# Performance work log

Hardware: AMD Instinct MI355X
Metric: run time of the kernel (lower is better)

Reference implementation:

```python
import jax, jax.numpy as jnp
import numpy as np

HEADS = 4
DIM_HEAD = 32
DIM = 128

def _layernorm(x, g, b, eps=1e-5):
    mu = x.mean(-1, keepdims=True)
    var = ((x - mu) ** 2).mean(-1, keepdims=True)
    return (x - mu) / jnp.sqrt(var + eps) * g + b

def setup_inputs() -> dict:
    key = jax.random.key(0)
    ks = jax.random.split(key, 12)
    d = {}
    d['q'] = jax.random.normal(ks[0], (1, 6, 8, 8, 16, 16, DIM), jnp.float32)
    d['k'] = jax.random.normal(ks[1], (1, 6, 8, 8, 6, 6, DIM), jnp.float32)
    d['v'] = jax.random.normal(ks[2], (1, 6, 8, 8, 6, 6, DIM), jnp.float32)
    d['skip'] = jax.random.normal(ks[3], (1, 8, 8, 16, 16, DIM), jnp.float32)
    inner = HEADS * DIM_HEAD
    # LayerNorm params for to_q/to_k/to_v pre-norms
    d['gq'] = jnp.ones((DIM,), jnp.float32); d['bq_ln'] = jnp.zeros((DIM,), jnp.float32)
    d['gk'] = jnp.ones((DIM,), jnp.float32); d['bk_ln'] = jnp.zeros((DIM,), jnp.float32)
    d['gv'] = jnp.ones((DIM,), jnp.float32); d['bv_ln'] = jnp.zeros((DIM,), jnp.float32)
    # Linear weights stored (in, out)
    d['Wq'] = jax.random.normal(ks[4], (DIM, inner), jnp.float32) * 0.02
    d['bq'] = jnp.zeros((inner,), jnp.float32)
    d['Wk'] = jax.random.normal(ks[5], (DIM, inner), jnp.float32) * 0.02
    d['bk'] = jnp.zeros((inner,), jnp.float32)
    d['Wv'] = jax.random.normal(ks[6], (DIM, inner), jnp.float32) * 0.02
    d['bv'] = jnp.zeros((inner,), jnp.float32)
    d['Wp'] = jax.random.normal(ks[7], (inner, DIM), jnp.float32) * 0.02
    d['bp'] = jnp.zeros((DIM,), jnp.float32)
    return d

def _window_flat(t):
    # (b n x y w1 w2 d) -> (b, x*y, n*w1*w2, d)
    b, n, gx, gy, wh, ww, d = t.shape
    t = jnp.transpose(t, (0, 2, 3, 1, 4, 5, 6))
    return t.reshape(b, gx * gy, n * wh * ww, d)

def reference(q, k, v, skip, gq, bq_ln, gk, bk_ln, gv, bv_ln, Wq, bq, Wk, bk, Wv, bv, Wp, bp):
    B, N, X, Y, W1, W2, D = q.shape
    scale = DIM_HEAD ** -0.5
    qf = _window_flat(q)  # (B, L, Qn, D), L = X*Y
    kf = _window_flat(k)  # (B, L, Kn, D)
    vf = _window_flat(v)
    L, Qn = qf.shape[1], qf.shape[2]
    Kn = kf.shape[2]
    qh = (_layernorm(qf, gq, bq_ln) @ Wq + bq).reshape(B, L, Qn, HEADS, DIM_HEAD)
    kh = (_layernorm(kf, gk, bk_ln) @ Wk + bk).reshape(B, L, Kn, HEADS, DIM_HEAD)
    vh = (_layernorm(vf, gv, bv_ln) @ Wv + bv).reshape(B, L, Kn, HEADS, DIM_HEAD)
    dot = jnp.einsum('blqhd,blkhd->bhlqk', qh, kh) * scale
    att = jax.nn.softmax(dot, axis=-1)
    a = jnp.einsum('bhlqk,blkhd->blqhd', att, vh).reshape(B, L, Qn, HEADS * DIM_HEAD)
    z = a @ Wp + bp  # (B, L, Qn, D)
    # back to (B, N, X, Y, W1, W2, D)
    z = z.reshape(B, X, Y, N, W1, W2, D)
    z = jnp.transpose(z, (0, 3, 1, 2, 4, 5, 6))
    z = z.mean(axis=1)  # pool over views -> (B, X, Y, W1, W2, D)
    return z + skip
```

## Files before the change

kernel.cpp:

```cpp
#include <hip/hip_runtime.h>

typedef __attribute__((ext_vector_type(8))) short bf16x8;
typedef __attribute__((ext_vector_type(4))) float f32x4;

__device__ __forceinline__ unsigned short f2bf(float f) {
  unsigned u = __builtin_bit_cast(unsigned, f);
  return (unsigned short)((u + 0x7fffu + ((u >> 16) & 1u)) >> 16);
}

__global__ __launch_bounds__(256) void prep_kernel(const float* __restrict__ W,
                                                   unsigned short* __restrict__ Wt) {
  int i = blockIdx.x * 256 + threadIdx.x;
  int k = i >> 7, n = i & 127;
  Wt[n * 128 + k] = f2bf(W[i]);
}

template <int WW>
__global__ __launch_bounds__(256) void ln_proj_kernel(
    const float* __restrict__ src,
    const float* __restrict__ gamma, const float* __restrict__ beta,
    const unsigned short* __restrict__ Wt,
    const float* __restrict__ bias, float outscale,
    unsigned short* __restrict__ dst) {
  __shared__ __align__(16) unsigned short xs[64][136];
  __shared__ __align__(16) unsigned short wsm[128][136];
  const int tid = threadIdx.x;
  const int base = blockIdx.x * 64;

  {
    const uint4* Wt4 = (const uint4*)Wt;
    for (int i = tid; i < 2048; i += 256)
      *(uint4*)&wsm[i >> 4][(i & 15) * 8] = Wt4[i];
  }

  const int tok = tid >> 2, part = tid & 3;
  {
    const float* x = src + (size_t)(base + tok) * 128 + part * 32;
    float v[32];
    float s = 0.f;
#pragma unroll
    for (int i = 0; i < 8; i++) {
      float4 f = ((const float4*)x)[i];
      v[4 * i] = f.x; v[4 * i + 1] = f.y; v[4 * i + 2] = f.z; v[4 * i + 3] = f.w;
      s += f.x + f.y + f.z + f.w;
    }
    s += __shfl_xor(s, 1); s += __shfl_xor(s, 2);
    const float mu = s * (1.f / 128.f);
    float vs = 0.f;
#pragma unroll
    for (int i = 0; i < 32; i++) { float d = v[i] - mu; vs += d * d; }
    vs += __shfl_xor(vs, 1); vs += __shfl_xor(vs, 2);
    const float rstd = rsqrtf(vs * (1.f / 128.f) + 1e-5f);
#pragma unroll
    for (int i = 0; i < 32; i++) {
      int d = part * 32 + i;
      xs[tok][d] = f2bf((v[i] - mu) * rstd * gamma[d] + beta[d]);
    }
  }
  __syncthreads();

  const int lane = tid & 63, wv = tid >> 6;
  const int lr = lane & 15, lg = lane >> 4;
  bf16x8 af[4];
#pragma unroll
  for (int ks = 0; ks < 4; ks++)
    af[ks] = *(const bf16x8*)&xs[wv * 16 + lr][ks * 32 + lg * 8];
  f32x4 acc[8];
#pragma unroll
  for (int nt = 0; nt < 8; nt++) {
    f32x4 a = {0.f, 0.f, 0.f, 0.f};
#pragma unroll
    for (int ks = 0; ks < 4; ks++) {
      bf16x8 bf = *(const bf16x8*)&wsm[nt * 16 + lr][ks * 32 + lg * 8];
      a = __builtin_amdgcn_mfma_f32_16x16x32_bf16(af[ks], bf, a, 0, 0, 0);
    }
    acc[nt] = a;
  }
  __syncthreads();
#pragma unroll
  for (int nt = 0; nt < 8; nt++) {
    const int n = nt * 16 + lr;
    const float b = bias[n];
#pragma unroll
    for (int rr = 0; rr < 4; rr++)
      xs[wv * 16 + lg * 4 + rr][n] = f2bf((acc[nt][rr] + b) * outscale);
  }
  __syncthreads();
  for (int i = tid; i < 1024; i += 256) {
    const int row = i >> 4, c8 = i & 15;
    const int sr = base + row;
    const int p = sr % WW;
    const int t1 = sr / WW;
    const int yy = t1 & 7;
    const int t2 = t1 >> 3;
    const int xx = t2 & 7;
    const int nn = t2 >> 3;
    const int dr = ((xx * 8 + yy) * 6 + nn) * WW + p;
    *(uint4*)(dst + (size_t)dr * 128 + c8 * 8) = *(const uint4*)&xs[row][c8 * 8];
  }
}

__global__ __launch_bounds__(512) void attn_kernel(
    const unsigned short* __restrict__ qh,
    const unsigned short* __restrict__ kh,
    const unsigned short* __restrict__ vh,
    float* __restrict__ abar) {
  __shared__ __align__(16) unsigned short Kl[224][40];
  __shared__ __align__(16) unsigned short Vt[32][232];
  __shared__ __align__(16) unsigned short P[8][16][248];
  const int tid = threadIdx.x;
  const int h = blockIdx.x, l = blockIdx.y;

  const unsigned short* kb = kh + (size_t)l * 216 * 128 + h * 32;
  for (int i = tid; i < 864; i += 512) {
    const int key = i >> 2, c = i & 3;
    *(uint4*)&Kl[key][c * 8] = *(const uint4*)&kb[(size_t)key * 128 + c * 8];
  }
  const unsigned short* vb = vh + (size_t)l * 216 * 128 + h * 32;
  for (int i = tid; i < 864; i += 512) {
    const int key = i >> 2, c = i & 3;
    uint4 d = *(const uint4*)&vb[(size_t)key * 128 + c * 8];
    const unsigned short* e = (const unsigned short*)&d;
#pragma unroll
    for (int j = 0; j < 8; j++) Vt[c * 8 + j][key] = e[j];
  }
  if (tid < 32) { uint4 z = {0, 0, 0, 0}; *(uint4*)&Vt[tid][216] = z; }
  __syncthreads();

  const int w = tid >> 6, lane = tid & 63;
  const int lr = lane & 15, lg = lane >> 4;

  for (int pt2 = 0; pt2 < 2; ++pt2) {
    const int pt = w * 2 + pt2;
    f32x4 acc[2] = {{0.f, 0.f, 0.f, 0.f}, {0.f, 0.f, 0.f, 0.f}};
#pragma unroll
    for (int wv = 0; wv < 6; ++wv) {
      const bf16x8 qf = *(const bf16x8*)
          &qh[((size_t)l * 1536 + wv * 256 + pt * 16 + lr) * 128 + h * 32 + lg * 8];

      f32x4 sc[14];
#pragma unroll
      for (int kt = 0; kt < 14; kt++) {
        bf16x8 kf = *(const bf16x8*)&Kl[kt * 16 + lr][lg * 8];
        f32x4 z = {0.f, 0.f, 0.f, 0.f};
        sc[kt] = __builtin_amdgcn_mfma_f32_16x16x32_bf16(kf, qf, z, 0, 0, 0);
      }
      if (lg >= 2) {
        sc[13][0] = -3e38f; sc[13][1] = -3e38f; sc[13][2] = -3e38f; sc[13][3] = -3e38f;
      }
      float sum = 0.f;
#pragma unroll
      for (int kt = 0; kt < 14; kt++)
#pragma unroll
        for (int rr = 0; rr < 4; rr++) {
          float e = __builtin_amdgcn_exp2f(sc[kt][rr]);
          sc[kt][rr] = e;
          sum += e;
        }
      sum += __shfl_xor(sum, 16);
      sum += __shfl_xor(sum, 32);
      const float inv = __builtin_amdgcn_rcpf(sum);

#pragma unroll
      for (int kt = 0; kt < 14; kt++) {
        unsigned r0, r1;
        asm("v_cvt_pk_bf16_f32 %0, %1, %2" : "=v"(r0) : "v"(sc[kt][0]), "v"(sc[kt][1]));
        asm("v_cvt_pk_bf16_f32 %0, %1, %2" : "=v"(r1) : "v"(sc[kt][2]), "v"(sc[kt][3]));
        uint2 wr; wr.x = r0; wr.y = r1;
        *(uint2*)&P[w][lr][kt * 16 + lg * 4] = wr;
      }

      f32x4 tmp[2] = {{0.f, 0.f, 0.f, 0.f}, {0.f, 0.f, 0.f, 0.f}};
#pragma unroll
      for (int s = 0; s < 7; s++) {
        bf16x8 pa = *(const bf16x8*)&P[w][lr][s * 32 + lg * 8];
#pragma unroll
        for (int nt = 0; nt < 2; nt++) {
          bf16x8 vf = *(const bf16x8*)&Vt[nt * 16 + lr][s * 32 + lg * 8];
          tmp[nt] = __builtin_amdgcn_mfma_f32_16x16x32_bf16(pa, vf, tmp[nt], 0, 0, 0);
        }
      }
#pragma unroll
      for (int rr = 0; rr < 4; rr++) {
        const float invq = __shfl(inv, lg * 4 + rr);
        acc[0][rr] += tmp[0][rr] * invq;
        acc[1][rr] += tmp[1][rr] * invq;
      }
    }
#pragma unroll
    for (int nt = 0; nt < 2; nt++)
#pragma unroll
      for (int rr = 0; rr < 4; rr++)
        abar[((size_t)l * 256 + pt * 16 + lg * 4 + rr) * 128 + h * 32 + nt * 16 + lr] =
            acc[nt][rr] * (1.f / 6.f);
  }
}

__global__ __launch_bounds__(256) void out_proj_kernel(
    const float* __restrict__ abar,
    const unsigned short* __restrict__ Wt,
    const float* __restrict__ bias,
    const float* __restrict__ skip,
    float* __restrict__ out) {
  __shared__ __align__(16) unsigned short xs[64][136];
  __shared__ __align__(16) unsigned short wsm[128][136];
  const int tid = threadIdx.x;
  const size_t base = (size_t)blockIdx.x * 64;
  {
    const uint4* Wt4 = (const uint4*)Wt;
    for (int i = tid; i < 2048; i += 256)
      *(uint4*)&wsm[i >> 4][(i & 15) * 8] = Wt4[i];
  }
  const int tok = tid >> 2, part = tid & 3;
  {
    const float* x = abar + (base + tok) * 128 + part * 32;
#pragma unroll
    for (int i = 0; i < 8; i++) {
      float4 f = ((const float4*)x)[i];
      unsigned short* o = &xs[tok][part * 32 + i * 4];
      o[0] = f2bf(f.x); o[1] = f2bf(f.y); o[2] = f2bf(f.z); o[3] = f2bf(f.w);
    }
  }
  __syncthreads();
  const int lane = tid & 63, wv = tid >> 6;
  const int lr = lane & 15, lg = lane >> 4;
  bf16x8 af[4];
#pragma unroll
  for (int ks = 0; ks < 4; ks++)
    af[ks] = *(const bf16x8*)&xs[wv * 16 + lr][ks * 32 + lg * 8];
#pragma unroll
  for (int nt = 0; nt < 8; nt++) {
    f32x4 a = {0.f, 0.f, 0.f, 0.f};
#pragma unroll
    for (int ks = 0; ks < 4; ks++) {
      bf16x8 bf = *(const bf16x8*)&wsm[nt * 16 + lr][ks * 32 + lg * 8];
      a = __builtin_amdgcn_mfma_f32_16x16x32_bf16(af[ks], bf, a, 0, 0, 0);
    }
    const int n = nt * 16 + lr;
    const float b = bias[n];
#pragma unroll
    for (int rr = 0; rr < 4; rr++) {
      const size_t row = base + wv * 16 + lg * 4 + rr;
      out[row * 128 + n] = a[rr] + b + skip[row * 128 + n];
    }
  }
}

extern "C" void kernel_launch(void* const* d_in, const int* in_sizes, int n_in,
                              void* d_out, int out_size, void* d_ws, size_t ws_size,
                              hipStream_t stream) {
  const float* q     = (const float*)d_in[0];
  const float* k     = (const float*)d_in[1];
  const float* v     = (const float*)d_in[2];
  const float* skip  = (const float*)d_in[3];
  const float* gq    = (const float*)d_in[4];
  const float* bq_ln = (const float*)d_in[5];
  const float* gk    = (const float*)d_in[6];
  const float* bk_ln = (const float*)d_in[7];
  const float* gv    = (const float*)d_in[8];
  const float* bv_ln = (const float*)d_in[9];
  const float* Wq    = (const float*)d_in[10];
  const float* bq    = (const float*)d_in[11];
  const float* Wk    = (const float*)d_in[12];
  const float* bk    = (const float*)d_in[13];
  const float* Wv    = (const float*)d_in[14];
  const float* bv    = (const float*)d_in[15];
  const float* Wp    = (const float*)d_in[16];
  const float* bp    = (const float*)d_in[17];

  char* w = (char*)d_ws;
  unsigned short* WtQ = (unsigned short*)(w);
  unsigned short* WtK = (unsigned short*)(w + 32768);
  unsigned short* WtV = (unsigned short*)(w + 65536);
  unsigned short* WtP = (unsigned short*)(w + 98304);
  unsigned short* qhb = (unsigned short*)(w + 131072);
  unsigned short* khb = (unsigned short*)(w + 131072 + 25165824);
  unsigned short* vhb = (unsigned short*)(w + 131072 + 25165824 + 3538944);
  float* abar         = (float*)(w + 131072 + 25165824 + 2 * 3538944);

  prep_kernel<<<64, 256, 0, stream>>>(Wq, WtQ);
  prep_kernel<<<64, 256, 0, stream>>>(Wk, WtK);
  prep_kernel<<<64, 256, 0, stream>>>(Wv, WtV);
  prep_kernel<<<64, 256, 0, stream>>>(Wp, WtP);

  const float scale = 0.17677669529663687f * 1.4426950408889634f;
  ln_proj_kernel<256><<<1536, 256, 0, stream>>>(q, gq, bq_ln, WtQ, bq, scale, qhb);
  ln_proj_kernel<36><<<216, 256, 0, stream>>>(k, gk, bk_ln, WtK, bk, 1.f, khb);
  ln_proj_kernel<36><<<216, 256, 0, stream>>>(v, gv, bv_ln, WtV, bv, 1.f, vhb);

  attn_kernel<<<dim3(4, 64), 512, 0, stream>>>(qhb, khb, vhb, abar);
  out_proj_kernel<<<256, 256, 0, stream>>>(abar, WtP, bp, skip, (float*)d_out);
}
```

Measured before the change: 92.24 us.

## Load LN/proj inputs straight into MFMA registers, enlarge blocks, prefetch Q in attention

After: 83.10 us. 9.9% less time.

```diff
diff --git a/kernel.cpp b/kernel.cpp
--- a/kernel.cpp
+++ b/kernel.cpp
@@ -6,6 +6,11 @@
 __device__ __forceinline__ unsigned short f2bf(float f) {
   unsigned u = __builtin_bit_cast(unsigned, f);
   return (unsigned short)((u + 0x7fffu + ((u >> 16) & 1u)) >> 16);
+}
+__device__ __forceinline__ unsigned pk2bf(float a, float b) {
+  unsigned r;
+  asm("v_cvt_pk_bf16_f32 %0, %1, %2" : "=v"(r) : "v"(a), "v"(b));
+  return r;
 }
 
 __global__ __launch_bounds__(256) void prep_kernel(const float* __restrict__ W,
@@ -16,55 +21,68 @@
 }
 
 template <int WW>
-__global__ __launch_bounds__(256) void ln_proj_kernel(
+__global__ __launch_bounds__(512, 4) void ln_proj_kernel(
     const float* __restrict__ src,
     const float* __restrict__ gamma, const float* __restrict__ beta,
     const unsigned short* __restrict__ Wt,
     const float* __restrict__ bias, float outscale,
     unsigned short* __restrict__ dst) {
-  __shared__ __align__(16) unsigned short xs[64][136];
+  __shared__ __align__(16) unsigned short xs[128][136];
   __shared__ __align__(16) unsigned short wsm[128][136];
   const int tid = threadIdx.x;
-  const int base = blockIdx.x * 64;
+  const int base = blockIdx.x * 128;
 
   {
     const uint4* Wt4 = (const uint4*)Wt;
-    for (int i = tid; i < 2048; i += 256)
+    for (int i = tid; i < 2048; i += 512)
       *(uint4*)&wsm[i >> 4][(i & 15) * 8] = Wt4[i];
   }
 
-  const int tok = tid >> 2, part = tid & 3;
+  const int w = tid >> 6, lane = tid & 63;
+  const int lr = lane & 15, lg = lane >> 4;
+  const int row = base + w * 16 + lr;
+
+  float v[32];
+  float s = 0.f;
   {
-    const float* x = src + (size_t)(base + tok) * 128 + part * 32;
-    float v[32];
-    float s = 0.f;
-#pragma unroll
-    for (int i = 0; i < 8; i++) {
-      float4 f = ((const float4*)x)[i];
-      v[4 * i] = f.x; v[4 * i + 1] = f.y; v[4 * i + 2] = f.z; v[4 * i + 3] = f.w;
-      s += f.x + f.y + f.z + f.w;
-    }
-    s += __shfl_xor(s, 1); s += __shfl_xor(s, 2);
-    const float mu = s * (1.f / 128.f);
-    float vs = 0.f;
-#pragma unroll
-    for (int i = 0; i < 32; i++) { float d = v[i] - mu; vs += d * d; }
-    vs += __shfl_xor(vs, 1); vs += __shfl_xor(vs, 2);
-    const float rstd = rsqrtf(vs * (1.f / 128.f) + 1e-5f);
-#pragma unroll
-    for (int i = 0; i < 32; i++) {
-      int d = part * 32 + i;
-      xs[tok][d] = f2bf((v[i] - mu) * rstd * gamma[d] + beta[d]);
-    }
+    const float* x = src + (size_t)row * 128 + lg * 8;
+#pragma unroll
+    for (int ks = 0; ks < 4; ks++)
+#pragma unroll
+      for (int j = 0; j < 2; j++) {
+        float4 f = *(const float4*)(x + ks * 32 + j * 4);
+        v[ks * 8 + j * 4 + 0] = f.x; v[ks * 8 + j * 4 + 1] = f.y;
+        v[ks * 8 + j * 4 + 2] = f.z; v[ks * 8 + j * 4 + 3] = f.w;
+        s += f.x + f.y + f.z + f.w;
+      }
+  }
+  s += __shfl_xor(s, 16); s += __shfl_xor(s, 32);
+  const float mu = s * (1.f / 128.f);
+  float vs = 0.f;
+#pragma unroll
+  for (int i = 0; i < 32; i++) { float d = v[i] - mu; vs += d * d; }
+  vs += __shfl_xor(vs, 16); vs += __shfl_xor(vs, 32);
+  const float rstd = rsqrtf(vs * (1.f / 128.f) + 1e-5f);
+
+  bf16x8 af[4];
+#pragma unroll
+  for (int ks = 0; ks < 4; ks++) {
+    unsigned pk[4];
+#pragma unroll
+    for (int j = 0; j < 2; j++) {
+      float4 g = *(const float4*)(gamma + ks * 32 + lg * 8 + j * 4);
+      float4 b = *(const float4*)(beta + ks * 32 + lg * 8 + j * 4);
+      float o0 = (v[ks * 8 + j * 4 + 0] - mu) * rstd * g.x + b.x;
+      float o1 = (v[ks * 8 + j * 4 + 1] - mu) * rstd * g.y + b.y;
+      float o2 = (v[ks * 8 + j * 4 + 2] - mu) * rstd * g.z + b.z;
+      float o3 = (v[ks * 8 + j * 4 + 3] - mu) * rstd * g.w + b.w;
+      pk[j * 2 + 0] = pk2bf(o0, o1);
+      pk[j * 2 + 1] = pk2bf(o2, o3);
+    }
+    af[ks] = __builtin_bit_cast(bf16x8, *(uint4*)pk);
   }
   __syncthreads();
 
-  const int lane = tid & 63, wv = tid >> 6;
-  const int lr = lane & 15, lg = lane >> 4;
-  bf16x8 af[4];
-#pragma unroll
-  for (int ks = 0; ks < 4; ks++)
-    af[ks] = *(const bf16x8*)&xs[wv * 16 + lr][ks * 32 + lg * 8];
   f32x4 acc[8];
 #pragma unroll
   for (int nt = 0; nt < 8; nt++) {
@@ -76,19 +94,18 @@
     }
     acc[nt] = a;
   }
-  __syncthreads();
 #pragma unroll
   for (int nt = 0; nt < 8; nt++) {
     const int n = nt * 16 + lr;
     const float b = bias[n];
 #pragma unroll
     for (int rr = 0; rr < 4; rr++)
-      xs[wv * 16 + lg * 4 + rr][n] = f2bf((acc[nt][rr] + b) * outscale);
+      xs[w * 16 + lg * 4 + rr][n] = f2bf((acc[nt][rr] + b) * outscale);
   }
   __syncthreads();
-  for (int i = tid; i < 1024; i += 256) {
-    const int row = i >> 4, c8 = i & 15;
-    const int sr = base + row;
+  for (int i = tid; i < 2048; i += 512) {
+    const int r = i >> 4, c8 = i & 15;
+    const int sr = base + r;
     const int p = sr % WW;
     const int t1 = sr / WW;
     const int yy = t1 & 7;
@@ -96,104 +113,107 @@
     const int xx = t2 & 7;
     const int nn = t2 >> 3;
     const int dr = ((xx * 8 + yy) * 6 + nn) * WW + p;
-    *(uint4*)(dst + (size_t)dr * 128 + c8 * 8) = *(const uint4*)&xs[row][c8 * 8];
-  }
-}
-
-__global__ __launch_bounds__(512) void attn_kernel(
+    *(uint4*)(dst + (size_t)dr * 128 + c8 * 8) = *(const uint4*)&xs[r][c8 * 8];
+  }
+}
+
+__global__ __launch_bounds__(1024) void attn_kernel(
     const unsigned short* __restrict__ qh,
     const unsigned short* __restrict__ kh,
     const unsigned short* __restrict__ vh,
     float* __restrict__ abar) {
   __shared__ __align__(16) unsigned short Kl[224][40];
   __shared__ __align__(16) unsigned short Vt[32][232];
-  __shared__ __align__(16) unsigned short P[8][16][248];
+  __shared__ __align__(16) unsigned short P[16][16][232];
   const int tid = threadIdx.x;
   const int h = blockIdx.x, l = blockIdx.y;
 
-  const unsigned short* kb = kh + (size_t)l * 216 * 128 + h * 32;
-  for (int i = tid; i < 864; i += 512) {
-    const int key = i >> 2, c = i & 3;
+  if (tid < 864) {
+    const unsigned short* kb = kh + (size_t)l * 216 * 128 + h * 32;
+    const int key = tid >> 2, c = tid & 3;
     *(uint4*)&Kl[key][c * 8] = *(const uint4*)&kb[(size_t)key * 128 + c * 8];
-  }
-  const unsigned short* vb = vh + (size_t)l * 216 * 128 + h * 32;
-  for (int i = tid; i < 864; i += 512) {
-    const int key = i >> 2, c = i & 3;
+    const unsigned short* vb = vh + (size_t)l * 216 * 128 + h * 32;
     uint4 d = *(const uint4*)&vb[(size_t)key * 128 + c * 8];
     const unsigned short* e = (const unsigned short*)&d;
 #pragma unroll
     for (int j = 0; j < 8; j++) Vt[c * 8 + j][key] = e[j];
   }
-  if (tid < 32) { uint4 z = {0, 0, 0, 0}; *(uint4*)&Vt[tid][216] = z; }
+  if (tid >= 960) { uint4 z = {0, 0, 0, 0}; *(uint4*)&Vt[tid - 960][216] = z; }
   __syncthreads();
 
   const int w = tid >> 6, lane = tid & 63;
   const int lr = lane & 15, lg = lane >> 4;
-
-  for (int pt2 = 0; pt2 < 2; ++pt2) {
-    const int pt = w * 2 + pt2;
-    f32x4 acc[2] = {{0.f, 0.f, 0.f, 0.f}, {0.f, 0.f, 0.f, 0.f}};
-#pragma unroll
-    for (int wv = 0; wv < 6; ++wv) {
-      const bf16x8 qf = *(const bf16x8*)
-          &qh[((size_t)l * 1536 + wv * 256 + pt * 16 + lr) * 128 + h * 32 + lg * 8];
-
-      f32x4 sc[14];
-#pragma unroll
-      for (int kt = 0; kt < 14; kt++) {
-        bf16x8 kf = *(const bf16x8*)&Kl[kt * 16 + lr][lg * 8];
-        f32x4 z = {0.f, 0.f, 0.f, 0.f};
-        sc[kt] = __builtin_amdgcn_mfma_f32_16x16x32_bf16(kf, qf, z, 0, 0, 0);
+  const int pt = w;
+
+  const unsigned short* qbase =
+      qh + ((size_t)l * 1536 + pt * 16 + lr) * 128 + h * 32 + lg * 8;
+
+  f32x4 acc[2] = {{0.f, 0.f, 0.f, 0.f}, {0.f, 0.f, 0.f, 0.f}};
+  bf16x8 qf = *(const bf16x8*)qbase;
+#pragma unroll
+  for (int wv = 0; wv < 6; ++wv) {
+    bf16x8 qnext;
+    if (wv < 5) qnext = *(const bf16x8*)(qbase + (size_t)(wv + 1) * 256 * 128);
+
+    f32x4 sc[14];
+    __builtin_amdgcn_s_setprio(1);
+#pragma unroll
+    for (int kt = 0; kt < 14; kt++) {
+      bf16x8 kf = *(const bf16x8*)&Kl[kt * 16 + lr][lg * 8];
+      f32x4 z = {0.f, 0.f, 0.f, 0.f};
+      sc[kt] = __builtin_amdgcn_mfma_f32_16x16x32_bf16(kf, qf, z, 0, 0, 0);
+    }
+    __builtin_amdgcn_s_setprio(0);
+    if (lg >= 2) {
+      sc[13][0] = -3e38f; sc[13][1] = -3e38f; sc[13][2] = -3e38f; sc[13][3] = -3e38f;
+    }
+    float sum = 0.f;
+#pragma unroll
+    for (int kt = 0; kt < 14; kt++)
+#pragma unroll
+      for (int rr = 0; rr < 4; rr++) {
+        float e = __builtin_amdgcn_exp2f(sc[kt][rr]);
+        sc[kt][rr] = e;
+        sum += e;
       }
-      if (lg >= 2) {
-        sc[13][0] = -3e38f; sc[13][1] = -3e38f; sc[13][2] = -3e38f; sc[13][3] = -3e38f;
+    sum += __shfl_xor(sum, 16);
+    sum += __shfl_xor(sum, 32);
+    const float inv = __builtin_amdgcn_rcpf(sum) * (1.f / 6.f);
+
+#pragma unroll
+    for (int kt = 0; kt < 14; kt++) {
+      uint2 wr;
+      wr.x = pk2bf(sc[kt][0], sc[kt][1]);
+      wr.y = pk2bf(sc[kt][2], sc[kt][3]);
+      *(uint2*)&P[w][lr][kt * 16 + lg * 4] = wr;
+    }
+
+    f32x4 tmp[2] = {{0.f, 0.f, 0.f, 0.f}, {0.f, 0.f, 0.f, 0.f}};
+    __builtin_amdgcn_s_setprio(1);
+#pragma unroll
+    for (int s = 0; s < 7; s++) {
+      bf16x8 pa = *(const bf16x8*)&P[w][lr][s * 32 + lg * 8];
+#pragma unroll
+      for (int nt = 0; nt < 2; nt++) {
+        bf16x8 vf = *(const bf16x8*)&Vt[nt * 16 + lr][s * 32 + lg * 8];
+        tmp[nt] = __builtin_amdgcn_mfma_f32_16x16x32_bf16(pa, vf, tmp[nt], 0, 0, 0);
       }
-      float sum = 0.f;
-#pragma unroll
-      for (int kt = 0; kt < 14; kt++)
-#pragma unroll
-        for (int rr = 0; rr < 4; rr++) {
-          float e = __builtin_amdgcn_exp2f(sc[kt][rr]);
-          sc[kt][rr] = e;
-          sum += e;
-        }
-      sum += __shfl_xor(sum, 16);
-      sum += __shfl_xor(sum, 32);
-      const float inv = __builtin_amdgcn_rcpf(sum);
-
-#pragma unroll
-      for (int kt = 0; kt < 14; kt++) {
-        unsigned r0, r1;
-        asm("v_cvt_pk_bf16_f32 %0, %1, %2" : "=v"(r0) : "v"(sc[kt][0]), "v"(sc[kt][1]));
-        asm("v_cvt_pk_bf16_f32 %0, %1, %2" : "=v"(r1) : "v"(sc[kt][2]), "v"(sc[kt][3]));
-        uint2 wr; wr.x = r0; wr.y = r1;
-        *(uint2*)&P[w][lr][kt * 16 + lg * 4] = wr;
-      }
-
-      f32x4 tmp[2] = {{0.f, 0.f, 0.f, 0.f}, {0.f, 0.f, 0.f, 0.f}};
-#pragma unroll
-      for (int s = 0; s < 7; s++) {
-        bf16x8 pa = *(const bf16x8*)&P[w][lr][s * 32 + lg * 8];
-#pragma unroll
-        for (int nt = 0; nt < 2; nt++) {
-          bf16x8 vf = *(const bf16x8*)&Vt[nt * 16 + lr][s * 32 + lg * 8];
-          tmp[nt] = __builtin_amdgcn_mfma_f32_16x16x32_bf16(pa, vf, tmp[nt], 0, 0, 0);
-        }
-      }
-#pragma unroll
-      for (int rr = 0; rr < 4; rr++) {
-        const float invq = __shfl(inv, lg * 4 + rr);
-        acc[0][rr] += tmp[0][rr] * invq;
-        acc[1][rr] += tmp[1][rr] * invq;
-      }
-    }
-#pragma unroll
-    for (int nt = 0; nt < 2; nt++)
-#pragma unroll
-      for (int rr = 0; rr < 4; rr++)
-        abar[((size_t)l * 256 + pt * 16 + lg * 4 + rr) * 128 + h * 32 + nt * 16 + lr] =
-            acc[nt][rr] * (1.f / 6.f);
-  }
+    }
+    __builtin_amdgcn_s_setprio(0);
+#pragma unroll
+    for (int rr = 0; rr < 4; rr++) {
+      const float invq = __shfl(inv, lg * 4 + rr);
+      acc[0][rr] += tmp[0][rr] * invq;
+      acc[1][rr] += tmp[1][rr] * invq;
+    }
+    qf = qnext;
+  }
+#pragma unroll
+  for (int nt = 0; nt < 2; nt++)
+#pragma unroll
+    for (int rr = 0; rr < 4; rr++)
+      abar[((size_t)l * 256 + pt * 16 + lg * 4 + rr) * 128 + h * 32 + nt * 16 + lr] =
+          acc[nt][rr];
 }
 
 __global__ __launch_bounds__(256) void out_proj_kernel(
@@ -202,7 +222,6 @@
     const float* __restrict__ bias,
     const float* __restrict__ skip,
     float* __restrict__ out) {
-  __shared__ __align__(16) unsigned short xs[64][136];
   __shared__ __align__(16) unsigned short wsm[128][136];
   const int tid = threadIdx.x;
   const size_t base = (size_t)blockIdx.x * 64;
@@ -211,23 +230,23 @@
     for (int i = tid; i < 2048; i += 256)
       *(uint4*)&wsm[i >> 4][(i & 15) * 8] = Wt4[i];
   }
-  const int tok = tid >> 2, part = tid & 3;
+  const int lane = tid & 63, w = tid >> 6;
+  const int lr = lane & 15, lg = lane >> 4;
+  const size_t row = base + w * 16 + lr;
+  bf16x8 af[4];
   {
-    const float* x = abar + (base + tok) * 128 + part * 32;
-#pragma unroll
-    for (int i = 0; i < 8; i++) {
-      float4 f = ((const float4*)x)[i];
-      unsigned short* o = &xs[tok][part * 32 + i * 4];
-      o[0] = f2bf(f.x); o[1] = f2bf(f.y); o[2] = f2bf(f.z); o[3] = f2bf(f.w);
+    const float* x = abar + row * 128 + lg * 8;
+#pragma unroll
+    for (int ks = 0; ks < 4; ks++) {
+      float4 f0 = *(const float4*)(x + ks * 32);
+      float4 f1 = *(const float4*)(x + ks * 32 + 4);
+      unsigned pk[4];
+      pk[0] = pk2bf(f0.x, f0.y); pk[1] = pk2bf(f0.z, f0.w);
+      pk[2] = pk2bf(f1.x, f1.y); pk[3] = pk2bf(f1.z, f1.w);
+      af[ks] = __builtin_bit_cast(bf16x8, *(uint4*)pk);
     }
   }
   __syncthreads();
-  const int lane = tid & 63, wv = tid >> 6;
-  const int lr = lane & 15, lg = lane >> 4;
-  bf16x8 af[4];
-#pragma unroll
-  for (int ks = 0; ks < 4; ks++)
-    af[ks] = *(const bf16x8*)&xs[wv * 16 + lr][ks * 32 + lg * 8];
 #pragma unroll
   for (int nt = 0; nt < 8; nt++) {
     f32x4 a = {0.f, 0.f, 0.f, 0.f};
@@ -240,8 +259,8 @@
     const float b = bias[n];
 #pragma unroll
     for (int rr = 0; rr < 4; rr++) {
-      const size_t row = base + wv * 16 + lg * 4 + rr;
-      out[row * 128 + n] = a[rr] + b + skip[row * 128 + n];
+      const size_t r = base + w * 16 + lg * 4 + rr;
+      out[r * 128 + n] = a[rr] + b + skip[r * 128 + n];
     }
   }
 }
@@ -284,10 +303,10 @@
   prep_kernel<<<64, 256, 0, stream>>>(Wp, WtP);
 
   const float scale = 0.17677669529663687f * 1.4426950408889634f;
-  ln_proj_kernel<256><<<1536, 256, 0, stream>>>(q, gq, bq_ln, WtQ, bq, scale, qhb);
-  ln_proj_kernel<36><<<216, 256, 0, stream>>>(k, gk, bk_ln, WtK, bk, 1.f, khb);
-  ln_proj_kernel<36><<<216, 256, 0, stream>>>(v, gv, bv_ln, WtV, bv, 1.f, vhb);
-
-  attn_kernel<<<dim3(4, 64), 512, 0, stream>>>(qhb, khb, vhb, abar);
+  ln_proj_kernel<256><<<768, 512, 0, stream>>>(q, gq, bq_ln, WtQ, bq, scale, qhb);
+  ln_proj_kernel<36><<<108, 512, 0, stream>>>(k, gk, bk_ln, WtK, bk, 1.f, khb);
+  ln_proj_kernel<36><<<108, 512, 0, stream>>>(v, gv, bv_ln, WtV, bv, 1.f, vhb);
+
+  attn_kernel<<<dim3(4, 64), 1024, 0, stream>>>(qhb, khb, vhb, abar);
   out_proj_kernel<<<256, 256, 0, stream>>>(abar, WtP, bp, skip, (float*)d_out);
 }
```
